# Kernel optimization log

Hardware: AMD Instinct MI355X
Metric: run time of the kernel (lower is better)

The kernel has to match this reference:

```python
import jax, jax.numpy as jnp
import numpy as np

D_MODEL = 512
NUM_HEADS = 8
HEAD_DIM = D_MODEL // NUM_HEADS


def setup_inputs() -> dict:
    key = jax.random.key(0)
    ks = jax.random.split(key, 11)
    N, S, D = 2, 4096, D_MODEL
    s = 1.0 / np.sqrt(D)
    return {
        "query": jax.random.normal(ks[0], (N, S, D), jnp.float32),
        "key": jax.random.normal(ks[1], (N, S, D), jnp.float32),
        "value": jax.random.normal(ks[2], (N, S, D), jnp.float32),
        "Wq": jax.random.normal(ks[3], (D, D), jnp.float32) * s,
        "bq": jnp.zeros((D,), jnp.float32),
        "Wk": jax.random.normal(ks[4], (D, D), jnp.float32) * s,
        "bk": jnp.zeros((D,), jnp.float32),
        "Wv": jax.random.normal(ks[5], (D, D), jnp.float32) * s,
        "bv": jnp.zeros((D,), jnp.float32),
        "Wo": jax.random.normal(ks[6], (D, D), jnp.float32) * s,
        "bo": jnp.zeros((D,), jnp.float32),
    }


def reference(query, key, value, Wq, bq, Wk, bk, Wv, bv, Wo, bo):
    N, S, D = query.shape
    H, Hd = NUM_HEADS, HEAD_DIM
    # Linear projections (torch Linear: x @ W.T + b), split heads -> [N,H,S,Hd]
    Q = (query @ Wq.T + bq).reshape(N, S, H, Hd).transpose(0, 2, 1, 3)
    K = (key @ Wk.T + bk).reshape(N, S, H, Hd).transpose(0, 2, 1, 3)
    V = (value @ Wv.T + bv).reshape(N, S, H, Hd).transpose(0, 2, 1, 3)
    scale = 1.0 / np.sqrt(Hd)
    energy = jnp.einsum("nhqd,nhkd->nhqk", Q, K) * scale  # [N,H,S,S]
    attention = jax.nn.softmax(energy, axis=-1)
    out = jnp.einsum("nhqk,nhkd->nhqd", attention, V)
    out = out.transpose(0, 2, 1, 3).reshape(N, S, D)
    return out @ Wo.T + bo
```

## Files before the change

kernel.cpp:

```cpp
#include <hip/hip_runtime.h>


#define SEQ 4096
#define PERHEAD 262144
#define CEXPF 0.18033688011112042f

typedef short bf16x8 __attribute__((ext_vector_type(8)));
typedef short bf16x4 __attribute__((ext_vector_type(4)));
typedef float f32x4 __attribute__((ext_vector_type(4)));
typedef unsigned short u16;
typedef unsigned int u32;

__device__ inline float bf2f(u16 h) {
    return __uint_as_float(((u32)h) << 16);
}
__device__ inline u16 f2bf(float f) {
    u32 u = __float_as_uint(f);
    u = (u + 0x7fffu + ((u >> 16) & 1u)) >> 16;
    return (u16)u;
}
__device__ inline u32 packtrunc(float lo, float hi) {
    return __builtin_amdgcn_perm(__float_as_uint(hi), __float_as_uint(lo),
                                 0x07060302u);
}
__device__ inline uint4 pack8(float4 a, float4 b) {
    uint4 r;
    r.x = (u32)f2bf(a.x) | ((u32)f2bf(a.y) << 16);
    r.y = (u32)f2bf(a.z) | ((u32)f2bf(a.w) << 16);
    r.z = (u32)f2bf(b.x) | ((u32)f2bf(b.y) << 16);
    r.w = (u32)f2bf(b.z) | ((u32)f2bf(b.w) << 16);
    return r;
}

__device__ inline int detect_f32(const void* W) {
    const int lane = threadIdx.x & 63;
    u16 uu = ((const u16*)W)[2 * lane];
    int e = (uu >> 7) & 0xFF;
    int plaus = (uu == 0) || (e >= 100 && e <= 132);
    unsigned long long m = __ballot(plaus);
    return (__popcll(m) >= 48) ? 0 : 1;
}

template <int A_BF16, int BM, int BN>
__device__ inline void gemm_dbuf(
    const void* __restrict__ Av, const void* __restrict__ Bv,
    const void* __restrict__ biasv, void* __restrict__ outv,
    int isf32, int mode, float scale, int m0, int n0,
    u16* As, u16* Bs)
{
    constexpr int MI = BM / 32;
    constexpr int NI = BN / 32;
    constexpr int TRA = 256 / BM;
    constexpr int CA = 32 / TRA;
    constexpr int NA = CA / 8;
    constexpr int TRB = 256 / BN;
    constexpr int CB = 32 / TRB;
    constexpr int NB = CB / 8;
    const int tid = threadIdx.x;
    const int wave = tid >> 6, lane = tid & 63, quad = lane >> 4, ln = lane & 15;
    const int qr = wave >> 1, qc = wave & 1;

    f32x4 acc[MI][NI];
#pragma unroll
    for (int i = 0; i < MI; i++)
#pragma unroll
        for (int j = 0; j < NI; j++) acc[i][j] = (f32x4){0.f, 0.f, 0.f, 0.f};

    const int arow = tid / TRA;
    const int acol = (tid % TRA) * CA;
    const int brow = tid / TRB;
    const int bcol = (tid % TRB) * CB;
    const u16*   A16 = (const u16*)Av;
    const float* A32 = (const float*)Av;
    const u16*   B16 = (const u16*)Bv;
    const float* B32 = (const float*)Bv;
    const size_t abase = (size_t)(m0 + arow) * 512 + acol;
    const size_t bbase = (size_t)(n0 + brow) * 512 + bcol;
    const int aoff = arow * 40 + acol;
    const int boff = brow * 40 + bcol;

    auto load_tiles = [&](int ka, uint4* aw, uint4* bw) {
        if (A_BF16 || !isf32) {
#pragma unroll
            for (int j = 0; j < NA; j++)
                aw[j] = *(const uint4*)(A16 + abase + ka + j * 8);
        } else {
            float4 fv[2 * NA];
#pragma unroll
            for (int j = 0; j < 2 * NA; j++)
                fv[j] = *(const float4*)(A32 + abase + ka + j * 4);
#pragma unroll
            for (int j = 0; j < NA; j++) aw[j] = pack8(fv[2 * j], fv[2 * j + 1]);
        }
        if (!isf32) {
#pragma unroll
            for (int j = 0; j < NB; j++)
                bw[j] = *(const uint4*)(B16 + bbase + ka + j * 8);
        } else {
            float4 fv[2 * NB];
#pragma unroll
            for (int j = 0; j < 2 * NB; j++)
                fv[j] = *(const float4*)(B32 + bbase + ka + j * 4);
#pragma unroll
            for (int j = 0; j < NB; j++) bw[j] = pack8(fv[2 * j], fv[2 * j + 1]);
        }
    };

    {
        uint4 aw[NA], bw[NB];
        load_tiles(0, aw, bw);
#pragma unroll
        for (int j = 0; j < NA; j++) *(uint4*)(As + aoff + j * 8) = aw[j];
#pragma unroll
        for (int j = 0; j < NB; j++) *(uint4*)(Bs + boff + j * 8) = bw[j];
    }
    __syncthreads();

    int ka = 32;
    for (int it = 0; it < 16; ++it) {
        uint4 aw[NA], bw[NB];
        load_tiles(ka, aw, bw);
        if (ka < 480) ka += 32;

        const u16* Ac = As + (it & 1) * (BM * 40);
        const u16* Bc = Bs + (it & 1) * (BN * 40);
        bf16x8 af[MI], bfr[NI];
#pragma unroll
        for (int mi = 0; mi < MI; mi++)
            af[mi] = *(const bf16x8*)(Ac + (qr * (BM / 2) + mi * 16 + ln) * 40 + quad * 8);
#pragma unroll
        for (int ni = 0; ni < NI; ni++)
            bfr[ni] = *(const bf16x8*)(Bc + (qc * (BN / 2) + ni * 16 + ln) * 40 + quad * 8);
#pragma unroll
        for (int mi = 0; mi < MI; mi++)
#pragma unroll
            for (int ni = 0; ni < NI; ni++)
                acc[mi][ni] = __builtin_amdgcn_mfma_f32_16x16x32_bf16(
                    af[mi], bfr[ni], acc[mi][ni], 0, 0, 0);

        u16* Aw = As + ((it + 1) & 1) * (BM * 40);
        u16* Bw = Bs + ((it + 1) & 1) * (BN * 40);
#pragma unroll
        for (int j = 0; j < NA; j++) *(uint4*)(Aw + aoff + j * 8) = aw[j];
#pragma unroll
        for (int j = 0; j < NB; j++) *(uint4*)(Bw + boff + j * 8) = bw[j];
        __syncthreads();
    }

    if (mode == 2 || (mode == 0 && isf32)) {
#pragma unroll
        for (int ni = 0; ni < NI; ni++) {
            const int col = n0 + qc * (BN / 2) + ni * 16 + ln;
            const float bvv = isf32 ? ((const float*)biasv)[col]
                                    : bf2f(((const u16*)biasv)[col]);
#pragma unroll
            for (int mi = 0; mi < MI; mi++) {
                const int row0 = m0 + qr * (BM / 2) + mi * 16 + quad * 4;
                float v0 = (acc[mi][ni][0] + bvv) * scale;
                float v1 = (acc[mi][ni][1] + bvv) * scale;
                float v2 = (acc[mi][ni][2] + bvv) * scale;
                float v3 = (acc[mi][ni][3] + bvv) * scale;
                if (mode == 0) {
                    const size_t idx = (size_t)row0 * 512 + col;
                    float* o = (float*)outv;
                    o[idx] = v0; o[idx + 512] = v1;
                    o[idx + 1024] = v2; o[idx + 1536] = v3;
                } else {
                    const int b = row0 >> 12, s = row0 & 4095;
                    const int h = col >> 6, hd = col & 63;
                    const int s6 = s & 63;
                    const int p = (s6 & 32) | ((s6 & 12) << 1) | ((s6 & 16) >> 2);
                    u16* o = (u16*)outv + (size_t)(b * 8 + h) * PERHEAD +
                             (size_t)hd * 4096 + (size_t)((s & ~63) + p);
                    uint2 pk;
                    pk.x = (u32)f2bf(v0) | ((u32)f2bf(v1) << 16);
                    pk.y = (u32)f2bf(v2) | ((u32)f2bf(v3) << 16);
                    *(uint2*)o = pk;
                }
            }
        }
    } else {
        u16* ls = As;
#pragma unroll
        for (int ni = 0; ni < NI; ni++) {
            const int coll = qc * (BN / 2) + ni * 16 + ln;
            const int col = n0 + coll;
            const float bvv = isf32 ? ((const float*)biasv)[col]
                                    : bf2f(((const u16*)biasv)[col]);
#pragma unroll
            for (int mi = 0; mi < MI; mi++) {
                const int rl = qr * (BM / 2) + mi * 16 + quad * 4;
#pragma unroll
                for (int r = 0; r < 4; r++)
                    ls[(rl + r) * 72 + coll] =
                        f2bf((acc[mi][ni][r] + bvv) * scale);
            }
        }
        __syncthreads();
        constexpr int TPR = 256 / BM;
        constexpr int CPT = BN / TPR;
        const int orow = tid / TPR;
        const int ocol = (tid % TPR) * CPT;
        const int rg = m0 + orow;
#pragma unroll
        for (int j = 0; j < CPT / 8; j++) {
            uint4 w = *(const uint4*)(ls + orow * 72 + ocol + j * 8);
            if (mode == 0) {
                *(uint4*)((u16*)outv + (size_t)rg * 512 + n0 + ocol + j * 8) = w;
            } else {
                const int b = rg >> 12, s = rg & 4095;
                const int h = n0 >> 6;
                *(uint4*)((u16*)outv + (size_t)(b * 8 + h) * PERHEAD +
                          (size_t)s * 64 + ocol + j * 8) = w;
            }
        }
    }
}

__global__ __launch_bounds__(256, 5) void qkv_proj(
    const void* __restrict__ q, const void* __restrict__ k, const void* __restrict__ v,
    const void* __restrict__ Wq, const void* __restrict__ Wk, const void* __restrict__ Wv,
    const void* __restrict__ bq, const void* __restrict__ bk, const void* __restrict__ bv,
    u16* __restrict__ Qh, u16* __restrict__ Kh, u16* __restrict__ Vt)
{
    __shared__ __align__(16) u16 As[2 * 128 * 40];
    __shared__ __align__(16) u16 Bs[2 * 64 * 40];
    const int gz = blockIdx.x + 8 * blockIdx.y;
    const int l = (gz & 7) * 64 + (gz >> 3);
    const int bx = l & 7;
    const int by = l >> 3;
    const int z = blockIdx.z;
    const void* Av = (z == 0) ? q : (z == 1) ? k : v;
    const void* Wz = (z == 0) ? Wq : (z == 1) ? Wk : Wv;
    const void* bz = (z == 0) ? bq : (z == 1) ? bk : bv;
    void* outv = (z == 0) ? (void*)Qh : (z == 1) ? (void*)Kh : (void*)Vt;
    const int mode = (z == 2) ? 2 : 1;
    const float scale = (z == 0) ? CEXPF : 1.0f;
    const int isf32 = detect_f32(Wz);
    gemm_dbuf<0, 128, 64>(Av, Wz, bz, outv, isf32, mode, scale,
                          by * 128, bx * 64, As, Bs);
}

__global__ __launch_bounds__(256, 4) void out_proj(
    const void* __restrict__ Av, const void* __restrict__ Wo,
    const void* __restrict__ bo, void* __restrict__ outv)
{
    __shared__ __align__(16) u16 As[2 * 64 * 40];
    __shared__ __align__(16) u16 Bs[2 * 64 * 40];
    const int g = blockIdx.x + 8 * blockIdx.y;
    const int l = (g & 7) * 128 + (g >> 3);
    const int bx = l & 7;
    const int by = l >> 3;
    const int isf32 = detect_f32(Wo);
    gemm_dbuf<1, 64, 64>(Av, Wo, bo, outv, isf32, 0, 1.0f,
                         by * 64, bx * 64, As, Bs);
}

__global__ __launch_bounds__(512) void attn_kernel(
    const u16* __restrict__ Q, const u16* __restrict__ K,
    const u16* __restrict__ Vt, u16* __restrict__ AO)
{
    __shared__ __align__(16) u16 SM[19456];

    const int tid = threadIdx.x;
    const int gw = tid >> 8;
    const int wq = (tid >> 6) & 3;
    const int lane = tid & 63, quad = lane >> 4, ln = lane & 15;
    const int gblk = blockIdx.x + 32 * blockIdx.y;
    const int lblk = (gblk & 7) * 64 + (gblk >> 3);
    const int bh = lblk >> 5;
    const int q0 = (lblk & 31) * 128;
    const size_t base = (size_t)bh * PERHEAD;

    bf16x8 qf[2][2];
#pragma unroll
    for (int qt = 0; qt < 2; qt++) {
        const uint4* qp = (const uint4*)(Q + base + (size_t)(q0 + wq * 32 + qt * 16 + ln) * 64);
        uint4 v0 = qp[quad], v1 = qp[4 + quad];
        qf[qt][0] = *(bf16x8*)&v0;
        qf[qt][1] = *(bf16x8*)&v1;
    }

    bf16x8 ones;
#pragma unroll
    for (int j = 0; j < 8; j++) ones[j] = (short)0x3F80;

    f32x4 oT[2][4];
    f32x4 lacc[2];
#pragma unroll
    for (int qt = 0; qt < 2; qt++) {
        lacc[qt] = (f32x4){0.f, 0.f, 0.f, 0.f};
#pragma unroll
        for (int mt = 0; mt < 4; mt++) oT[qt][mt] = (f32x4){0.f, 0.f, 0.f, 0.f};
    }

    const int tid2 = tid & 255;
    const int srowK = tid2 >> 3, scK = (tid2 & 7) * 8;
    const int srowV = tid2 >> 2, scV = (tid2 & 3) * 8;
    const uint4* Kg = (const uint4*)(K + base + (size_t)(gw * 2048 + srowK) * 64 + scK);
    const uint4* Vg = (const uint4*)(Vt + base + (size_t)srowV * 4096 + gw * 2048 + scV);
    const int kloff = srowK * 72 + scK;
    const int vloff = srowV * 40 + scV;

    {
        uint4 a = Kg[0], c = Vg[0];
        Kg += 256; Vg += 4;
        *(uint4*)(SM + (gw * 2 + 0) * 2304 + kloff) = a;
        *(uint4*)(SM + 9216 + (gw * 2 + 0) * 2560 + vloff) = c;
    }
    __syncthreads();

    for (int it = 0; it < 64; ++it) {
        const u16* Kc = SM + (gw * 2 + (it & 1)) * 2304;
        const u16* Vc = SM + 9216 + (gw * 2 + (it & 1)) * 2560;

        uint4 pa = Kg[0], pc = Vg[0];
        Kg += 256; Vg += 4;

        f32x4 s[2][2];
        __builtin_amdgcn_s_setprio(1);
#pragma unroll
        for (int t = 0; t < 2; t++)
#pragma unroll
            for (int kt = 0; kt < 2; kt++) {
                bf16x8 kf = *(const bf16x8*)(Kc + (kt * 16 + ln) * 72 + t * 32 + quad * 8);
#pragma unroll
                for (int qt = 0; qt < 2; qt++) {
                    if (t == 0)
                        s[qt][kt] = __builtin_amdgcn_mfma_f32_16x16x32_bf16(
                            kf, qf[qt][0], (f32x4){0.f, 0.f, 0.f, 0.f}, 0, 0, 0);
                    else
                        s[qt][kt] = __builtin_amdgcn_mfma_f32_16x16x32_bf16(
                            kf, qf[qt][1], s[qt][kt], 0, 0, 0);
                }
            }
        __builtin_amdgcn_s_setprio(0);

        bf16x8 pf[2];
#pragma unroll
        for (int qt = 0; qt < 2; qt++) {
            float e0 = __builtin_amdgcn_exp2f(s[qt][0][0]);
            float e1 = __builtin_amdgcn_exp2f(s[qt][0][1]);
            float e2 = __builtin_amdgcn_exp2f(s[qt][0][2]);
            float e3 = __builtin_amdgcn_exp2f(s[qt][0][3]);
            float f0 = __builtin_amdgcn_exp2f(s[qt][1][0]);
            float f1 = __builtin_amdgcn_exp2f(s[qt][1][1]);
            float f2 = __builtin_amdgcn_exp2f(s[qt][1][2]);
            float f3 = __builtin_amdgcn_exp2f(s[qt][1][3]);
            u32 w0 = packtrunc(e0, e1), w1 = packtrunc(e2, e3);
            u32 w2 = packtrunc(f0, f1), w3 = packtrunc(f2, f3);
            uint4 pk = {w0, w1, w2, w3};
            pf[qt] = *(bf16x8*)&pk;
        }

        __builtin_amdgcn_s_setprio(1);
#pragma unroll
        for (int qt = 0; qt < 2; qt++)
            lacc[qt] = __builtin_amdgcn_mfma_f32_16x16x32_bf16(
                ones, pf[qt], lacc[qt], 0, 0, 0);

#pragma unroll
        for (int mt = 0; mt < 4; mt++) {
            bf16x8 vf = *(const bf16x8*)(Vc + (mt * 16 + ln) * 40 + quad * 8);
#pragma unroll
            for (int qt = 0; qt < 2; qt++)
                oT[qt][mt] = __builtin_amdgcn_mfma_f32_16x16x32_bf16(
                    vf, pf[qt], oT[qt][mt], 0, 0, 0);
        }
        __builtin_amdgcn_s_setprio(0);

        *(uint4*)(SM + (gw * 2 + ((it + 1) & 1)) * 2304 + kloff) = pa;
        *(uint4*)(SM + 9216 + (gw * 2 + ((it + 1) & 1)) * 2560 + vloff) = pc;
        __syncthreads();
    }

    float* Xch = (float*)SM;
    if (gw == 1) {
#pragma unroll
        for (int qt = 0; qt < 2; qt++) {
#pragma unroll
            for (int mt = 0; mt < 4; mt++)
#pragma unroll
                for (int r = 0; r < 4; r++)
                    Xch[(((wq * 2 + qt) * 4 + mt) * 16 + quad * 4 + r) * 17 + ln] =
                        oT[qt][mt][r];
            if (quad == 0)
                Xch[8704 + (wq * 2 + qt) * 16 + ln] = lacc[qt][0];
        }
    }
    __syncthreads();
    if (gw == 0) {
        const int b = bh >> 3, h = bh & 7;
#pragma unroll
        for (int qt = 0; qt < 2; qt++) {
            const float l2 = Xch[8704 + (wq * 2 + qt) * 16 + ln];
            const float inv = 1.0f / (lacc[qt][0] + l2);
            const int qrow = q0 + wq * 32 + qt * 16 + ln;
            u16* op = AO + (size_t)(b * 4096 + qrow) * 512 + h * 64 + quad * 4;
#pragma unroll
            for (int mt = 0; mt < 4; mt++) {
                float o0 = oT[qt][mt][0] +
                    Xch[(((wq * 2 + qt) * 4 + mt) * 16 + quad * 4 + 0) * 17 + ln];
                float o1 = oT[qt][mt][1] +
                    Xch[(((wq * 2 + qt) * 4 + mt) * 16 + quad * 4 + 1) * 17 + ln];
                float o2 = oT[qt][mt][2] +
                    Xch[(((wq * 2 + qt) * 4 + mt) * 16 + quad * 4 + 2) * 17 + ln];
                float o3 = oT[qt][mt][3] +
                    Xch[(((wq * 2 + qt) * 4 + mt) * 16 + quad * 4 + 3) * 17 + ln];
                uint2 pk;
                pk.x = (u32)f2bf(o0 * inv) | ((u32)f2bf(o1 * inv) << 16);
                pk.y = (u32)f2bf(o2 * inv) | ((u32)f2bf(o3 * inv) << 16);
                *(uint2*)(op + mt * 16) = pk;
            }
        }
    }
}

extern "C" void kernel_launch(void* const* d_in, const int* in_sizes, int n_in,
                              void* d_out, int out_size, void* d_ws, size_t ws_size,
                              hipStream_t stream)
{
    (void)in_sizes; (void)n_in; (void)out_size; (void)ws_size;
    const void* q  = d_in[0];
    const void* k  = d_in[1];
    const void* v  = d_in[2];
    const void* Wq = d_in[3];
    const void* bq = d_in[4];
    const void* Wk = d_in[5];
    const void* bk = d_in[6];
    const void* Wv = d_in[7];
    const void* bv = d_in[8];
    const void* Wo = d_in[9];
    const void* bo = d_in[10];

    u16* ws = (u16*)d_ws;
    u16* Kh = ws;
    u16* Vt = ws + 4194304;
    u16* AO = ws + 8388608;
    u16* Qh = (u16*)d_out;

    qkv_proj<<<dim3(8, 64, 3), 256, 0, stream>>>(q, k, v, Wq, Wk, Wv,
                                                 bq, bk, bv, Qh, Kh, Vt);
    attn_kernel<<<dim3(32, 16), 512, 0, stream>>>(Qh, Kh, Vt, AO);
    out_proj<<<dim3(8, 128), 256, 0, stream>>>(AO, Wo, bo, d_out);
}
```

Before: 241.3 us.

## Stage full weight slab in LDS and stream A fragments directly from global

Both projection GEMMs are restructured. Each block now loads its entire 64x512 weight slab into LDS once, and each wave streams its own 32 rows of A from global memory straight into MFMA fragments. This removes the per-k-step double-buffered LDS staging and the barrier inside the main loop. The output projection moves to 128-row tiles with half as many blocks. The cost is about 65 KB of LDS per block, which limits occupancy to around 2 blocks per CU, and A reads from global are uncoalesced and have no latency hiding.

Result: slower. 281.1 us (+16.5%).

```diff
diff --git a/kernel.cpp b/kernel.cpp
--- a/kernel.cpp
+++ b/kernel.cpp
@@ -41,125 +41,88 @@
     return (__popcll(m) >= 48) ? 0 : 1;
 }
 
-template <int A_BF16, int BM, int BN>
-__device__ inline void gemm_dbuf(
+template <int A_BF16>
+__device__ inline void gemm_nobar(
     const void* __restrict__ Av, const void* __restrict__ Bv,
     const void* __restrict__ biasv, void* __restrict__ outv,
-    int isf32, int mode, float scale, int m0, int n0,
-    u16* As, u16* Bs)
+    int isf32, int mode, float scale, int m0, int n0, u16* Bs)
 {
-    constexpr int MI = BM / 32;
-    constexpr int NI = BN / 32;
-    constexpr int TRA = 256 / BM;
-    constexpr int CA = 32 / TRA;
-    constexpr int NA = CA / 8;
-    constexpr int TRB = 256 / BN;
-    constexpr int CB = 32 / TRB;
-    constexpr int NB = CB / 8;
     const int tid = threadIdx.x;
-    const int wave = tid >> 6, lane = tid & 63, quad = lane >> 4, ln = lane & 15;
-    const int qr = wave >> 1, qc = wave & 1;
-
-    f32x4 acc[MI][NI];
-#pragma unroll
-    for (int i = 0; i < MI; i++)
-#pragma unroll
-        for (int j = 0; j < NI; j++) acc[i][j] = (f32x4){0.f, 0.f, 0.f, 0.f};
-
-    const int arow = tid / TRA;
-    const int acol = (tid % TRA) * CA;
-    const int brow = tid / TRB;
-    const int bcol = (tid % TRB) * CB;
+    const int w = tid >> 6, lane = tid & 63, quad = lane >> 4, ln = lane & 15;
+
+    {
+        const int row = tid >> 2;
+        const int seg = (tid & 3) * 128;
+        u16* dst = Bs + row * 520 + seg;
+        if (!isf32) {
+            const u16* src = (const u16*)Bv + (size_t)(n0 + row) * 512 + seg;
+#pragma unroll
+            for (int j = 0; j < 16; j++)
+                *(uint4*)(dst + j * 8) = *(const uint4*)(src + j * 8);
+        } else {
+            const float* src = (const float*)Bv + (size_t)(n0 + row) * 512 + seg;
+#pragma unroll
+            for (int j = 0; j < 16; j++) {
+                float4 f0 = *(const float4*)(src + j * 8);
+                float4 f1 = *(const float4*)(src + j * 8 + 4);
+                *(uint4*)(dst + j * 8) = pack8(f0, f1);
+            }
+        }
+    }
+    __syncthreads();
+
+    f32x4 acc[2][4];
+#pragma unroll
+    for (int i = 0; i < 2; i++)
+#pragma unroll
+        for (int j = 0; j < 4; j++) acc[i][j] = (f32x4){0.f, 0.f, 0.f, 0.f};
+
     const u16*   A16 = (const u16*)Av;
     const float* A32 = (const float*)Av;
-    const u16*   B16 = (const u16*)Bv;
-    const float* B32 = (const float*)Bv;
-    const size_t abase = (size_t)(m0 + arow) * 512 + acol;
-    const size_t bbase = (size_t)(n0 + brow) * 512 + bcol;
-    const int aoff = arow * 40 + acol;
-    const int boff = brow * 40 + bcol;
-
-    auto load_tiles = [&](int ka, uint4* aw, uint4* bw) {
-        if (A_BF16 || !isf32) {
-#pragma unroll
-            for (int j = 0; j < NA; j++)
-                aw[j] = *(const uint4*)(A16 + abase + ka + j * 8);
-        } else {
-            float4 fv[2 * NA];
-#pragma unroll
-            for (int j = 0; j < 2 * NA; j++)
-                fv[j] = *(const float4*)(A32 + abase + ka + j * 4);
-#pragma unroll
-            for (int j = 0; j < NA; j++) aw[j] = pack8(fv[2 * j], fv[2 * j + 1]);
-        }
-        if (!isf32) {
-#pragma unroll
-            for (int j = 0; j < NB; j++)
-                bw[j] = *(const uint4*)(B16 + bbase + ka + j * 8);
-        } else {
-            float4 fv[2 * NB];
-#pragma unroll
-            for (int j = 0; j < 2 * NB; j++)
-                fv[j] = *(const float4*)(B32 + bbase + ka + j * 4);
-#pragma unroll
-            for (int j = 0; j < NB; j++) bw[j] = pack8(fv[2 * j], fv[2 * j + 1]);
-        }
-    };
-
-    {
-        uint4 aw[NA], bw[NB];
-        load_tiles(0, aw, bw);
-#pragma unroll
-        for (int j = 0; j < NA; j++) *(uint4*)(As + aoff + j * 8) = aw[j];
-#pragma unroll
-        for (int j = 0; j < NB; j++) *(uint4*)(Bs + boff + j * 8) = bw[j];
-    }
+    const int arow = m0 + w * 32 + ln;
+
+#pragma unroll
+    for (int kk = 0; kk < 512; kk += 32) {
+        bf16x8 af[2];
+#pragma unroll
+        for (int st = 0; st < 2; st++) {
+            const size_t off = (size_t)(arow + st * 16) * 512 + kk + quad * 8;
+            if (A_BF16 || !isf32) {
+                uint4 t = *(const uint4*)(A16 + off);
+                af[st] = *(bf16x8*)&t;
+            } else {
+                float4 f0 = *(const float4*)(A32 + off);
+                float4 f1 = *(const float4*)(A32 + off + 4);
+                uint4 t = pack8(f0, f1);
+                af[st] = *(bf16x8*)&t;
+            }
+        }
+        bf16x8 bfr[4];
+#pragma unroll
+        for (int ns = 0; ns < 4; ns++)
+            bfr[ns] = *(const bf16x8*)(Bs + (ns * 16 + ln) * 520 + kk + quad * 8);
+#pragma unroll
+        for (int st = 0; st < 2; st++)
+#pragma unroll
+            for (int ns = 0; ns < 4; ns++)
+                acc[st][ns] = __builtin_amdgcn_mfma_f32_16x16x32_bf16(
+                    af[st], bfr[ns], acc[st][ns], 0, 0, 0);
+    }
+
     __syncthreads();
-
-    int ka = 32;
-    for (int it = 0; it < 16; ++it) {
-        uint4 aw[NA], bw[NB];
-        load_tiles(ka, aw, bw);
-        if (ka < 480) ka += 32;
-
-        const u16* Ac = As + (it & 1) * (BM * 40);
-        const u16* Bc = Bs + (it & 1) * (BN * 40);
-        bf16x8 af[MI], bfr[NI];
-#pragma unroll
-        for (int mi = 0; mi < MI; mi++)
-            af[mi] = *(const bf16x8*)(Ac + (qr * (BM / 2) + mi * 16 + ln) * 40 + quad * 8);
-#pragma unroll
-        for (int ni = 0; ni < NI; ni++)
-            bfr[ni] = *(const bf16x8*)(Bc + (qc * (BN / 2) + ni * 16 + ln) * 40 + quad * 8);
-#pragma unroll
-        for (int mi = 0; mi < MI; mi++)
-#pragma unroll
-            for (int ni = 0; ni < NI; ni++)
-                acc[mi][ni] = __builtin_amdgcn_mfma_f32_16x16x32_bf16(
-                    af[mi], bfr[ni], acc[mi][ni], 0, 0, 0);
-
-        u16* Aw = As + ((it + 1) & 1) * (BM * 40);
-        u16* Bw = Bs + ((it + 1) & 1) * (BN * 40);
-#pragma unroll
-        for (int j = 0; j < NA; j++) *(uint4*)(Aw + aoff + j * 8) = aw[j];
-#pragma unroll
-        for (int j = 0; j < NB; j++) *(uint4*)(Bw + boff + j * 8) = bw[j];
-        __syncthreads();
-    }
-
     if (mode == 2 || (mode == 0 && isf32)) {
 #pragma unroll
-        for (int ni = 0; ni < NI; ni++) {
-            const int col = n0 + qc * (BN / 2) + ni * 16 + ln;
+        for (int ns = 0; ns < 4; ns++) {
+            const int col = n0 + ns * 16 + ln;
             const float bvv = isf32 ? ((const float*)biasv)[col]
                                     : bf2f(((const u16*)biasv)[col]);
 #pragma unroll
-            for (int mi = 0; mi < MI; mi++) {
-                const int row0 = m0 + qr * (BM / 2) + mi * 16 + quad * 4;
-                float v0 = (acc[mi][ni][0] + bvv) * scale;
-                float v1 = (acc[mi][ni][1] + bvv) * scale;
-                float v2 = (acc[mi][ni][2] + bvv) * scale;
-                float v3 = (acc[mi][ni][3] + bvv) * scale;
+            for (int st = 0; st < 2; st++) {
+                const int row0 = m0 + w * 32 + st * 16 + quad * 4;
+                float v0 = (acc[st][ns][0] + bvv) * scale;
+                float v1 = (acc[st][ns][1] + bvv) * scale;
+                float v2 = (acc[st][ns][2] + bvv) * scale;
+                float v3 = (acc[st][ns][3] + bvv) * scale;
                 if (mode == 0) {
                     const size_t idx = (size_t)row0 * 512 + col;
                     float* o = (float*)outv;
@@ -180,51 +143,48 @@
             }
         }
     } else {
-        u16* ls = As;
-#pragma unroll
-        for (int ni = 0; ni < NI; ni++) {
-            const int coll = qc * (BN / 2) + ni * 16 + ln;
+        u16* ls = Bs;
+#pragma unroll
+        for (int ns = 0; ns < 4; ns++) {
+            const int coll = ns * 16 + ln;
             const int col = n0 + coll;
             const float bvv = isf32 ? ((const float*)biasv)[col]
                                     : bf2f(((const u16*)biasv)[col]);
 #pragma unroll
-            for (int mi = 0; mi < MI; mi++) {
-                const int rl = qr * (BM / 2) + mi * 16 + quad * 4;
+            for (int st = 0; st < 2; st++) {
+                const int rl = w * 32 + st * 16 + quad * 4;
 #pragma unroll
                 for (int r = 0; r < 4; r++)
                     ls[(rl + r) * 72 + coll] =
-                        f2bf((acc[mi][ni][r] + bvv) * scale);
+                        f2bf((acc[st][ns][r] + bvv) * scale);
             }
         }
         __syncthreads();
-        constexpr int TPR = 256 / BM;
-        constexpr int CPT = BN / TPR;
-        const int orow = tid / TPR;
-        const int ocol = (tid % TPR) * CPT;
+        const int orow = tid >> 1;
+        const int ocol = (tid & 1) * 32;
         const int rg = m0 + orow;
 #pragma unroll
-        for (int j = 0; j < CPT / 8; j++) {
-            uint4 w = *(const uint4*)(ls + orow * 72 + ocol + j * 8);
+        for (int j = 0; j < 4; j++) {
+            uint4 wv = *(const uint4*)(ls + orow * 72 + ocol + j * 8);
             if (mode == 0) {
-                *(uint4*)((u16*)outv + (size_t)rg * 512 + n0 + ocol + j * 8) = w;
+                *(uint4*)((u16*)outv + (size_t)rg * 512 + n0 + ocol + j * 8) = wv;
             } else {
                 const int b = rg >> 12, s = rg & 4095;
                 const int h = n0 >> 6;
                 *(uint4*)((u16*)outv + (size_t)(b * 8 + h) * PERHEAD +
-                          (size_t)s * 64 + ocol + j * 8) = w;
-            }
-        }
-    }
-}
-
-__global__ __launch_bounds__(256, 5) void qkv_proj(
+                          (size_t)s * 64 + ocol + j * 8) = wv;
+            }
+        }
+    }
+}
+
+__global__ __launch_bounds__(256, 2) void qkv_proj(
     const void* __restrict__ q, const void* __restrict__ k, const void* __restrict__ v,
     const void* __restrict__ Wq, const void* __restrict__ Wk, const void* __restrict__ Wv,
     const void* __restrict__ bq, const void* __restrict__ bk, const void* __restrict__ bv,
     u16* __restrict__ Qh, u16* __restrict__ Kh, u16* __restrict__ Vt)
 {
-    __shared__ __align__(16) u16 As[2 * 128 * 40];
-    __shared__ __align__(16) u16 Bs[2 * 64 * 40];
+    __shared__ __align__(16) u16 Bs[64 * 520];
     const int gz = blockIdx.x + 8 * blockIdx.y;
     const int l = (gz & 7) * 64 + (gz >> 3);
     const int bx = l & 7;
@@ -237,23 +197,22 @@
     const int mode = (z == 2) ? 2 : 1;
     const float scale = (z == 0) ? CEXPF : 1.0f;
     const int isf32 = detect_f32(Wz);
-    gemm_dbuf<0, 128, 64>(Av, Wz, bz, outv, isf32, mode, scale,
-                          by * 128, bx * 64, As, Bs);
-}
-
-__global__ __launch_bounds__(256, 4) void out_proj(
+    gemm_nobar<0>(Av, Wz, bz, outv, isf32, mode, scale,
+                  by * 128, bx * 64, Bs);
+}
+
+__global__ __launch_bounds__(256, 2) void out_proj(
     const void* __restrict__ Av, const void* __restrict__ Wo,
     const void* __restrict__ bo, void* __restrict__ outv)
 {
-    __shared__ __align__(16) u16 As[2 * 64 * 40];
-    __shared__ __align__(16) u16 Bs[2 * 64 * 40];
+    __shared__ __align__(16) u16 Bs[64 * 520];
     const int g = blockIdx.x + 8 * blockIdx.y;
-    const int l = (g & 7) * 128 + (g >> 3);
+    const int l = (g & 7) * 64 + (g >> 3);
     const int bx = l & 7;
     const int by = l >> 3;
     const int isf32 = detect_f32(Wo);
-    gemm_dbuf<1, 64, 64>(Av, Wo, bo, outv, isf32, 0, 1.0f,
-                         by * 64, bx * 64, As, Bs);
+    gemm_nobar<1>(Av, Wo, bo, outv, isf32, 0, 1.0f,
+                  by * 128, bx * 64, Bs);
 }
 
 __global__ __launch_bounds__(512) void attn_kernel(
@@ -442,5 +401,5 @@
     qkv_proj<<<dim3(8, 64, 3), 256, 0, stream>>>(q, k, v, Wq, Wk, Wv,
                                                  bq, bk, bv, Qh, Kh, Vt);
     attn_kernel<<<dim3(32, 16), 512, 0, stream>>>(Qh, Kh, Vt, AO);
-    out_proj<<<dim3(8, 128), 256, 0, stream>>>(AO, Wo, bo, d_out);
-}
+    out_proj<<<dim3(8, 64), 256, 0, stream>>>(AO, Wo, bo, d_out);
+}
```
